# Optimization experiments

Hardware: AMD Instinct MI355X
Metric: run time of the kernel (lower is better)

## Reference

```python
import jax, jax.numpy as jnp
import numpy as np

N = 40000      # nodes
E = 640000     # edges (before self-loops)
F_IN = 32      # num_node_features
H = 8          # n_heads
C = 16         # hidden_channels
G = 1000       # graphs in batch
M = 256        # MLP_neurons
NEG_SLOPE = 0.2


def setup_inputs() -> dict:
    key = jax.random.key(0)
    ks = jax.random.split(key, 24)
    d = {}
    d["x"] = jax.random.normal(ks[0], (N, F_IN), jnp.float32)
    d["edge_index"] = jax.random.randint(ks[1], (2, E), 0, N, dtype=jnp.int32)
    d["batch"] = jnp.sort(jax.random.randint(ks[2], (N,), 0, G, dtype=jnp.int32))
    dims = [F_IN, H * C, H * C]
    k = 3
    for i in range(3):
        fin = dims[i]
        s = 1.0 / np.sqrt(fin)
        d[f"W{i}"] = jax.random.normal(ks[k], (fin, H * C), jnp.float32) * s; k += 1
        d[f"b{i}"] = jnp.zeros((H * C,), jnp.float32)
        d[f"as{i}"] = jax.random.normal(ks[k], (H, C), jnp.float32) * (1.0 / np.sqrt(C)); k += 1
        d[f"ad{i}"] = jax.random.normal(ks[k], (H, C), jnp.float32) * (1.0 / np.sqrt(C)); k += 1
    d["fW0"] = jax.random.normal(ks[k], (H * C, M), jnp.float32) * (1.0 / np.sqrt(H * C)); k += 1
    d["fb0"] = jnp.zeros((M,), jnp.float32)
    d["fW1"] = jax.random.normal(ks[k], (M, M), jnp.float32) * (1.0 / np.sqrt(M)); k += 1
    d["fb1"] = jnp.zeros((M,), jnp.float32)
    d["oW"] = jax.random.normal(ks[k], (M, 2), jnp.float32) * (1.0 / np.sqrt(M)); k += 1
    d["ob"] = jnp.zeros((2,), jnp.float32)
    return d


def _gat_layer(x, W, b, a_src, a_dst, src, dst):
    # x: [N, Fin] -> h: [N, H, C]
    h = (x @ W).reshape(N, H, C)
    al_src = jnp.einsum('nhc,hc->nh', h, a_src)   # [N, H]
    al_dst = jnp.einsum('nhc,hc->nh', h, a_dst)   # [N, H]
    # edge-wise attention logits (gather), LeakyReLU
    e = jax.nn.leaky_relu(al_src[src] + al_dst[dst], NEG_SLOPE)  # [E', H]
    # softmax over incoming edges of each dst node
    emax = jax.ops.segment_max(e, dst, num_segments=N)           # [N, H]
    ex = jnp.exp(e - emax[dst])
    denom = jax.ops.segment_sum(ex, dst, num_segments=N)         # [N, H]
    alpha = ex / denom[dst]
    # weighted scatter-aggregation of source features
    out = jax.ops.segment_sum(alpha[:, :, None] * h[src], dst, num_segments=N)  # [N, H, C]
    return out.reshape(N, H * C) + b


def reference(x, edge_index, batch, W0, b0, as0, ad0, W1, b1, as1, ad1,
              W2, b2, as2, ad2, fW0, fb0, fW1, fb1, oW, ob):
    # PyG GATConv adds self-loops by default
    loops = jnp.arange(N, dtype=edge_index.dtype)
    src = jnp.concatenate([edge_index[0], loops])
    dst = jnp.concatenate([edge_index[1], loops])
    h = x
    for (W, b, a_s, a_d) in ((W0, b0, as0, ad0), (W1, b1, as1, ad1), (W2, b2, as2, ad2)):
        h = jax.nn.relu(_gat_layer(h, W, b, a_s, a_d, src, dst))
    # global mean pool per graph
    sums = jax.ops.segment_sum(h, batch, num_segments=G)                    # [G, H*C]
    cnts = jax.ops.segment_sum(jnp.ones((N,), h.dtype), batch, num_segments=G)
    g = sums / jnp.maximum(cnts, 1.0)[:, None]
    # MLP head (dropout is identity in eval mode)
    g = jax.nn.relu(g @ fW0 + fb0)
    g = jax.nn.relu(g @ fW1 + fb1)
    return g @ oW + ob
```

## Files before the change

kernel.cpp:

```cpp
#include <hip/hip_runtime.h>
#include <hip/hip_fp16.h>
#include <math.h>

#define NN 40000
#define EE 640000
#define EP 680000
#define FIN0 32
#define HC 128
#define GG 1000
#define MM 256
#define SCAN_BLOCKS ((NN + 255) / 256)


__global__ void hist_kernel(const int* __restrict__ ei, int* __restrict__ deg,
                            int* __restrict__ rank) {
    int idx = blockIdx.x * 256 + threadIdx.x;
    if (idx >= EP) return;
    int d = (idx < EE) ? ei[EE + idx] : (idx - EE);
    rank[idx] = atomicAdd(&deg[d], 1);
}

__global__ __launch_bounds__(256) void scan_partial(const int* __restrict__ deg,
                                                    int* __restrict__ part) {
    int b = blockIdx.x, t = threadIdx.x;
    int i = b * 256 + t;
    int v = (i < NN) ? deg[i] : 0;
#pragma unroll
    for (int d = 1; d < 64; d <<= 1) v += __shfl_xor(v, d);
    __shared__ int ws[4];
    if ((t & 63) == 0) ws[t >> 6] = v;
    __syncthreads();
    if (t == 0) part[b] = ws[0] + ws[1] + ws[2] + ws[3];
}

__global__ __launch_bounds__(256) void scan_final(const int* __restrict__ deg,
                                                  const int* __restrict__ part,
                                                  int* __restrict__ offs) {
    int b = blockIdx.x, t = threadIdx.x;
    __shared__ int sbase;
    if (t < 64) {
        int s = 0;
        for (int l = t; l < b; l += 64) s += part[l];
#pragma unroll
        for (int d = 1; d < 64; d <<= 1) s += __shfl_xor(s, d);
        if (t == 0) sbase = s;
    }
    int i = b * 256 + t;
    int v = (i < NN) ? deg[i] : 0;
    __shared__ int tmp[256];
    tmp[t] = v;
    __syncthreads();
    for (int st = 1; st < 256; st <<= 1) {
        int add = (t >= st) ? tmp[t - st] : 0;
        __syncthreads();
        tmp[t] += add;
        __syncthreads();
    }
    int excl = tmp[t] - v + sbase;
    if (i < NN) offs[i] = excl;
    if (i == NN - 1) offs[NN] = excl + v;
}

__global__ void scatter_kernel(const int* __restrict__ ei, const int* __restrict__ offs,
                               const int* __restrict__ rank, int* __restrict__ esrc) {
    int idx = blockIdx.x * 256 + threadIdx.x;
    if (idx >= EP) return;
    int s, d;
    if (idx < EE) { s = ei[idx]; d = ei[EE + idx]; } else { s = idx - EE; d = s; }
    esrc[offs[d] + rank[idx]] = s;
}


template <int FIN>
__global__ __launch_bounds__(256) void proj_kernel(const float* __restrict__ X,
                                                   const float* __restrict__ W,
                                                   const float* __restrict__ a_src,
                                                   const float* __restrict__ a_dst,
                                                   __half* __restrict__ H2,
                                                   float* __restrict__ als,
                                                   float* __restrict__ ald) {
    constexpr int KT = 32;
    static_assert(FIN % KT == 0, "FIN % KT");
    __shared__ float xs[KT][68];
    __shared__ float ws[KT][128];
    int t = threadIdx.x;
    int node0 = blockIdx.x * 64;
    int nt = t & 15;
    int ct = t >> 4;
    float acc[4][8];
#pragma unroll
    for (int i = 0; i < 4; i++)
#pragma unroll
        for (int j = 0; j < 8; j++) acc[i][j] = 0.f;

    for (int kk = 0; kk < FIN; kk += KT) {
#pragma unroll
        for (int r = 0; r < (64 * KT) / 256; r++) {
            int idx = r * 256 + t;
            int n = idx / KT, k = idx % KT;
            xs[k][n] = X[(node0 + n) * FIN + kk + k];
        }
#pragma unroll
        for (int r = 0; r < (KT * 128) / 256; r++) {
            int idx = r * 256 + t;
            int k = idx >> 7, c = idx & 127;
            ws[k][c] = W[(kk + k) * 128 + c];
        }
        __syncthreads();
#pragma unroll
        for (int k = 0; k < KT; k++) {
            const float4 xv = *(const float4*)(&xs[k][4 * nt]);
            const float4 wa = *(const float4*)(&ws[k][8 * ct]);
            const float4 wb = *(const float4*)(&ws[k][8 * ct + 4]);
            float xr[4] = {xv.x, xv.y, xv.z, xv.w};
            float wr[8] = {wa.x, wa.y, wa.z, wa.w, wb.x, wb.y, wb.z, wb.w};
#pragma unroll
            for (int i = 0; i < 4; i++)
#pragma unroll
                for (int j = 0; j < 8; j++) acc[i][j] = fmaf(xr[i], wr[j], acc[i][j]);
        }
        __syncthreads();
    }
#pragma unroll
    for (int i = 0; i < 4; i++) {
        int n = node0 + 4 * nt + i;
        __half2 p0 = __floats2half2_rn(acc[i][0], acc[i][1]);
        __half2 p1 = __floats2half2_rn(acc[i][2], acc[i][3]);
        __half2 p2 = __floats2half2_rn(acc[i][4], acc[i][5]);
        __half2 p3 = __floats2half2_rn(acc[i][6], acc[i][7]);
        uint4 pk;
        pk.x = *(unsigned*)&p0; pk.y = *(unsigned*)&p1;
        pk.z = *(unsigned*)&p2; pk.w = *(unsigned*)&p3;
        *(uint4*)(&H2[(size_t)n * HC + 8 * ct]) = pk;
    }
    float sa[4] = {0.f, 0.f, 0.f, 0.f}, da[4] = {0.f, 0.f, 0.f, 0.f};
#pragma unroll
    for (int j = 0; j < 8; j++) {
        float av = a_src[ct * 8 + j];
        float dv = a_dst[ct * 8 + j];
#pragma unroll
        for (int i = 0; i < 4; i++) {
            sa[i] = fmaf(acc[i][j], av, sa[i]);
            da[i] = fmaf(acc[i][j], dv, da[i]);
        }
    }
#pragma unroll
    for (int i = 0; i < 4; i++) {
        sa[i] += __shfl_xor(sa[i], 16);
        da[i] += __shfl_xor(da[i], 16);
    }
    if ((ct & 1) == 0) {
        int head = ct >> 1;
#pragma unroll
        for (int i = 0; i < 4; i++) {
            int n = node0 + 4 * nt + i;
            als[n * 8 + head] = sa[i];
            ald[n * 8 + head] = da[i];
        }
    }
}


__global__ __launch_bounds__(256) void agg_kernel(const __half* __restrict__ H2,
                                                  const float* __restrict__ als,
                                                  const float* __restrict__ ald,
                                                  const int* __restrict__ offs,
                                                  const int* __restrict__ esrc,
                                                  const float* __restrict__ bias,
                                                  float* __restrict__ OUT) {
    int t = threadIdx.x;
    int n = blockIdx.x * 4 + (t >> 6);
    int t6 = t & 63;
    int c8 = t6 & 15;
    int slot = (t6 >> 4) & 3;
    int hd = c8 >> 1;
    int beg = offs[n], end = offs[n + 1];
    float ad = ald[n * 8 + hd];
    float acc[8] = {0.f, 0.f, 0.f, 0.f, 0.f, 0.f, 0.f, 0.f};
    float denom = 0.f;
    const float4* H4 = (const float4*)H2;

    int p = beg + slot;
    int s_cur = 0; float al_cur = 0.f;
    if (p < end) {
        s_cur = esrc[p];
        al_cur = als[s_cur * 8 + hd];
    }
#pragma unroll 2
    while (p < end) {
        int pn = p + 4;
        int s_nxt = 0;
        if (pn < end) s_nxt = esrc[pn];
        float x = al_cur + ad;
        x = (x > 0.f) ? x : 0.2f * x;
        float w = __expf(x);
        float4 r = H4[(size_t)s_cur * 16 + c8];
        float al_nxt = 0.f;
        if (pn < end) al_nxt = als[s_nxt * 8 + hd];
        __half2 h0 = *(__half2*)&r.x;
        __half2 h1 = *(__half2*)&r.y;
        __half2 h2 = *(__half2*)&r.z;
        __half2 h3 = *(__half2*)&r.w;
        float2 f0 = __half22float2(h0);
        float2 f1 = __half22float2(h1);
        float2 f2 = __half22float2(h2);
        float2 f3 = __half22float2(h3);
        acc[0] = fmaf(w, f0.x, acc[0]); acc[1] = fmaf(w, f0.y, acc[1]);
        acc[2] = fmaf(w, f1.x, acc[2]); acc[3] = fmaf(w, f1.y, acc[3]);
        acc[4] = fmaf(w, f2.x, acc[4]); acc[5] = fmaf(w, f2.y, acc[5]);
        acc[6] = fmaf(w, f3.x, acc[6]); acc[7] = fmaf(w, f3.y, acc[7]);
        denom += w;
        s_cur = s_nxt; al_cur = al_nxt;
        p = pn;
    }
#pragma unroll
    for (int j = 0; j < 8; j++) {
        acc[j] += __shfl_xor(acc[j], 16);
        acc[j] += __shfl_xor(acc[j], 32);
    }
    denom += __shfl_xor(denom, 16);
    denom += __shfl_xor(denom, 32);
    if (slot == 0 && t6 < 16) {
        float inv = 1.0f / denom;
        const float4 ba = ((const float4*)bias)[2 * c8];
        const float4 bb = ((const float4*)bias)[2 * c8 + 1];
        float4 o0, o1;
        o0.x = fmaxf(fmaf(acc[0], inv, ba.x), 0.f);
        o0.y = fmaxf(fmaf(acc[1], inv, ba.y), 0.f);
        o0.z = fmaxf(fmaf(acc[2], inv, ba.z), 0.f);
        o0.w = fmaxf(fmaf(acc[3], inv, ba.w), 0.f);
        o1.x = fmaxf(fmaf(acc[4], inv, bb.x), 0.f);
        o1.y = fmaxf(fmaf(acc[5], inv, bb.y), 0.f);
        o1.z = fmaxf(fmaf(acc[6], inv, bb.z), 0.f);
        o1.w = fmaxf(fmaf(acc[7], inv, bb.w), 0.f);
        ((float4*)OUT)[(size_t)n * 32 + 2 * c8]     = o0;
        ((float4*)OUT)[(size_t)n * 32 + 2 * c8 + 1] = o1;
    }
}


__global__ __launch_bounds__(256) void mlp_fused(const float* __restrict__ B,
                                                 const int* __restrict__ batch,
                                                 const float* __restrict__ fW0,
                                                 const float* __restrict__ fb0,
                                                 const float* __restrict__ fW1,
                                                 const float* __restrict__ fb1,
                                                 const float* __restrict__ oW,
                                                 const float* __restrict__ ob,
                                                 float* __restrict__ out) {
    __shared__ int lo[3];
    __shared__ float rows[2][128];
    __shared__ float g1s[2][256];
    __shared__ float g2s[2][256];
    int t = threadIdx.x;
    int g0 = blockIdx.x * 2;
    if (t < 3) {
        int target = g0 + t;
        int a = 0, b = NN;
        while (a < b) { int mid = (a + b) >> 1; if (batch[mid] < target) a = mid + 1; else b = mid; }
        lo[t] = a;
    }
    __syncthreads();
    {
        int j = t >> 7, c = t & 127;
        int s0 = lo[j], s1 = lo[j + 1];
        float s = 0.f;
        float p0 = 0.f, p1 = 0.f, p2 = 0.f, p3 = 0.f;
        int n = s0;
        for (; n + 3 < s1; n += 4) {
            p0 += B[(size_t)n * 128 + c];
            p1 += B[(size_t)(n + 1) * 128 + c];
            p2 += B[(size_t)(n + 2) * 128 + c];
            p3 += B[(size_t)(n + 3) * 128 + c];
        }
        for (; n < s1; n++) s += B[(size_t)n * 128 + c];
        s += (p0 + p1) + (p2 + p3);
        rows[j][c] = s / fmaxf((float)(s1 - s0), 1.0f);
    }
    __syncthreads();
    float a0 = 0.f, a1 = 0.f;
#pragma unroll 8
    for (int k = 0; k < 128; k++) {
        float w = fW0[k * 256 + t];
        a0 = fmaf(rows[0][k], w, a0);
        a1 = fmaf(rows[1][k], w, a1);
    }
    float b0v = fb0[t];
    g1s[0][t] = fmaxf(a0 + b0v, 0.f);
    g1s[1][t] = fmaxf(a1 + b0v, 0.f);
    __syncthreads();
    a0 = 0.f; a1 = 0.f;
#pragma unroll 8
    for (int k = 0; k < 256; k++) {
        float w = fW1[k * 256 + t];
        a0 = fmaf(g1s[0][k], w, a0);
        a1 = fmaf(g1s[1][k], w, a1);
    }
    float b1v = fb1[t];
    g2s[0][t] = fmaxf(a0 + b1v, 0.f);
    g2s[1][t] = fmaxf(a1 + b1v, 0.f);
    __syncthreads();
    if (t < 64) {
        int jj = t >> 5, l = t & 31;
        float p0 = 0.f, p1 = 0.f;
#pragma unroll
        for (int k = l; k < 256; k += 32) {
            float v = g2s[jj][k];
            p0 = fmaf(v, oW[k * 2 + 0], p0);
            p1 = fmaf(v, oW[k * 2 + 1], p1);
        }
#pragma unroll
        for (int d = 1; d < 32; d <<= 1) {
            p0 += __shfl_xor(p0, d);
            p1 += __shfl_xor(p1, d);
        }
        if (l == 0) {
            out[(g0 + jj) * 2 + 0] = p0 + ob[0];
            out[(g0 + jj) * 2 + 1] = p1 + ob[1];
        }
    }
}


extern "C" void kernel_launch(void* const* d_in, const int* in_sizes, int n_in,
                              void* d_out, int out_size, void* d_ws, size_t ws_size,
                              hipStream_t stream) {
    const float* x    = (const float*)d_in[0];
    const int* ei     = (const int*)d_in[1];
    const int* batch  = (const int*)d_in[2];
    const float* W[3]   = {(const float*)d_in[3], (const float*)d_in[7],  (const float*)d_in[11]};
    const float* bs[3]  = {(const float*)d_in[4], (const float*)d_in[8],  (const float*)d_in[12]};
    const float* asr[3] = {(const float*)d_in[5], (const float*)d_in[9],  (const float*)d_in[13]};
    const float* adt[3] = {(const float*)d_in[6], (const float*)d_in[10], (const float*)d_in[14]};
    const float* fW0 = (const float*)d_in[15];
    const float* fb0 = (const float*)d_in[16];
    const float* fW1 = (const float*)d_in[17];
    const float* fb1 = (const float*)d_in[18];
    const float* oW  = (const float*)d_in[19];
    const float* ob  = (const float*)d_in[20];
    float* out = (float*)d_out;

    char* base = (char*)d_ws;
    size_t off = 0;
    auto alloc = [&](size_t bytes) -> void* {
        void* p = base + off;
        off += (bytes + 255) & ~(size_t)255;
        return p;
    };
    int* deg    = (int*)alloc((size_t)NN * 4);
    int* offs   = (int*)alloc((size_t)(NN + 1) * 4);
    int* part   = (int*)alloc((size_t)SCAN_BLOCKS * 4);
    int* rank   = (int*)alloc((size_t)EP * 4);
    int* esrc   = (int*)alloc((size_t)EP * 4);
    __half* H2  = (__half*)alloc((size_t)NN * HC * 2);
    float* B    = (float*)alloc((size_t)NN * HC * 4);
    float* als  = (float*)alloc((size_t)NN * 8 * 4);
    float* ald  = (float*)alloc((size_t)NN * 8 * 4);

    hipMemsetAsync(deg, 0, (size_t)NN * 4, stream);

    hist_kernel<<<(EP + 255) / 256, 256, 0, stream>>>(ei, deg, rank);
    scan_partial<<<SCAN_BLOCKS, 256, 0, stream>>>(deg, part);
    scan_final<<<SCAN_BLOCKS, 256, 0, stream>>>(deg, part, offs);
    scatter_kernel<<<(EP + 255) / 256, 256, 0, stream>>>(ei, offs, rank, esrc);

    const float* cur = x;
    for (int l = 0; l < 3; l++) {
        if (l == 0) proj_kernel<FIN0><<<NN / 64, 256, 0, stream>>>(cur, W[l], asr[l], adt[l], H2, als, ald);
        else        proj_kernel<HC><<<NN / 64, 256, 0, stream>>>(cur, W[l], asr[l], adt[l], H2, als, ald);
        agg_kernel<<<NN / 4, 256, 0, stream>>>(H2, als, ald, offs, esrc, bs[l], B);
        cur = B;
    }
    mlp_fused<<<GG / 2, 256, 0, stream>>>(B, batch, fW0, fb0, fW1, fb1, oW, ob, out);
}
```

Baseline: 319.7 us.

## Use fp16 MFMA for hidden-layer projections and fuse layer-0 proj with histogram

Replaces the fp32 FMA projection for layers 1 and 2 with an MFMA 16x16x32 fp16 kernel. It reads fp16 activations written by the aggregation kernel, which now emits half output for the first two layers, and uses pre-transposed fp16 weights. The layer-0 projection, the degree histogram and the weight transpose/convert are merged into one prep kernel launch, so independent work overlaps and there are fewer launches. This lowers the precision of the intermediate activations and weights to fp16 and halves the activation bytes written and read between layers.

```diff
diff --git a/kernel.cpp b/kernel.cpp
--- a/kernel.cpp
+++ b/kernel.cpp
@@ -10,81 +10,53 @@
 #define GG 1000
 #define MM 256
 #define SCAN_BLOCKS ((NN + 255) / 256)
-
-
-__global__ void hist_kernel(const int* __restrict__ ei, int* __restrict__ deg,
-                            int* __restrict__ rank) {
-    int idx = blockIdx.x * 256 + threadIdx.x;
-    if (idx >= EP) return;
-    int d = (idx < EE) ? ei[EE + idx] : (idx - EE);
-    rank[idx] = atomicAdd(&deg[d], 1);
-}
-
-__global__ __launch_bounds__(256) void scan_partial(const int* __restrict__ deg,
-                                                    int* __restrict__ part) {
-    int b = blockIdx.x, t = threadIdx.x;
-    int i = b * 256 + t;
-    int v = (i < NN) ? deg[i] : 0;
-#pragma unroll
-    for (int d = 1; d < 64; d <<= 1) v += __shfl_xor(v, d);
-    __shared__ int ws[4];
-    if ((t & 63) == 0) ws[t >> 6] = v;
-    __syncthreads();
-    if (t == 0) part[b] = ws[0] + ws[1] + ws[2] + ws[3];
-}
-
-__global__ __launch_bounds__(256) void scan_final(const int* __restrict__ deg,
-                                                  const int* __restrict__ part,
-                                                  int* __restrict__ offs) {
-    int b = blockIdx.x, t = threadIdx.x;
-    __shared__ int sbase;
-    if (t < 64) {
-        int s = 0;
-        for (int l = t; l < b; l += 64) s += part[l];
-#pragma unroll
-        for (int d = 1; d < 64; d <<= 1) s += __shfl_xor(s, d);
-        if (t == 0) sbase = s;
-    }
-    int i = b * 256 + t;
-    int v = (i < NN) ? deg[i] : 0;
-    __shared__ int tmp[256];
-    tmp[t] = v;
-    __syncthreads();
-    for (int st = 1; st < 256; st <<= 1) {
-        int add = (t >= st) ? tmp[t - st] : 0;
-        __syncthreads();
-        tmp[t] += add;
-        __syncthreads();
-    }
-    int excl = tmp[t] - v + sbase;
-    if (i < NN) offs[i] = excl;
-    if (i == NN - 1) offs[NN] = excl + v;
-}
-
-__global__ void scatter_kernel(const int* __restrict__ ei, const int* __restrict__ offs,
-                               const int* __restrict__ rank, int* __restrict__ esrc) {
-    int idx = blockIdx.x * 256 + threadIdx.x;
-    if (idx >= EP) return;
-    int s, d;
-    if (idx < EE) { s = ei[idx]; d = ei[EE + idx]; } else { s = idx - EE; d = s; }
-    esrc[offs[d] + rank[idx]] = s;
-}
-
-
-template <int FIN>
-__global__ __launch_bounds__(256) void proj_kernel(const float* __restrict__ X,
-                                                   const float* __restrict__ W,
+#define PROJ0_BLOCKS (NN / 64)
+#define HIST_BLOCKS ((EP + 255) / 256)
+#define PADH 136
+
+typedef _Float16 f16x8 __attribute__((ext_vector_type(8)));
+typedef float f32x4 __attribute__((ext_vector_type(4)));
+
+
+__global__ __launch_bounds__(256) void prep_kernel(const float* __restrict__ X,
+                                                   const float* __restrict__ W0,
                                                    const float* __restrict__ a_src,
                                                    const float* __restrict__ a_dst,
                                                    __half* __restrict__ H2,
                                                    float* __restrict__ als,
-                                                   float* __restrict__ ald) {
-    constexpr int KT = 32;
-    static_assert(FIN % KT == 0, "FIN % KT");
-    __shared__ float xs[KT][68];
-    __shared__ float ws[KT][128];
+                                                   float* __restrict__ ald,
+                                                   const int* __restrict__ ei,
+                                                   int* __restrict__ deg,
+                                                   int* __restrict__ rank,
+                                                   const float* __restrict__ W1,
+                                                   const float* __restrict__ W2,
+                                                   __half* __restrict__ Wt1,
+                                                   __half* __restrict__ Wt2) {
     int t = threadIdx.x;
-    int node0 = blockIdx.x * 64;
+    int b = blockIdx.x;
+    if (b >= PROJ0_BLOCKS && b < PROJ0_BLOCKS + HIST_BLOCKS) {
+        int idx = (b - PROJ0_BLOCKS) * 256 + t;
+        if (idx < EP) {
+            int d = (idx < EE) ? ei[EE + idx] : (idx - EE);
+            rank[idx] = atomicAdd(&deg[d], 1);
+        }
+        return;
+    }
+    if (b >= PROJ0_BLOCKS + HIST_BLOCKS) {
+        int l = b - (PROJ0_BLOCKS + HIST_BLOCKS);
+        const float* Wsrc = (l == 0) ? W1 : W2;
+        __half* Wd = (l == 0) ? Wt1 : Wt2;
+#pragma unroll 8
+        for (int r = 0; r < 64; r++) {
+            int idx = r * 256 + t;
+            int k = idx >> 7, c = idx & 127;
+            Wd[c * 128 + k] = __float2half(Wsrc[idx]);
+        }
+        return;
+    }
+    __shared__ float xs[32][68];
+    __shared__ float ws[32][128];
+    int node0 = b * 64;
     int nt = t & 15;
     int ct = t >> 4;
     float acc[4][8];
@@ -92,34 +64,30 @@
     for (int i = 0; i < 4; i++)
 #pragma unroll
         for (int j = 0; j < 8; j++) acc[i][j] = 0.f;
-
-    for (int kk = 0; kk < FIN; kk += KT) {
-#pragma unroll
-        for (int r = 0; r < (64 * KT) / 256; r++) {
-            int idx = r * 256 + t;
-            int n = idx / KT, k = idx % KT;
-            xs[k][n] = X[(node0 + n) * FIN + kk + k];
-        }
-#pragma unroll
-        for (int r = 0; r < (KT * 128) / 256; r++) {
-            int idx = r * 256 + t;
-            int k = idx >> 7, c = idx & 127;
-            ws[k][c] = W[(kk + k) * 128 + c];
-        }
-        __syncthreads();
-#pragma unroll
-        for (int k = 0; k < KT; k++) {
-            const float4 xv = *(const float4*)(&xs[k][4 * nt]);
-            const float4 wa = *(const float4*)(&ws[k][8 * ct]);
-            const float4 wb = *(const float4*)(&ws[k][8 * ct + 4]);
-            float xr[4] = {xv.x, xv.y, xv.z, xv.w};
-            float wr[8] = {wa.x, wa.y, wa.z, wa.w, wb.x, wb.y, wb.z, wb.w};
-#pragma unroll
-            for (int i = 0; i < 4; i++)
-#pragma unroll
-                for (int j = 0; j < 8; j++) acc[i][j] = fmaf(xr[i], wr[j], acc[i][j]);
-        }
-        __syncthreads();
+#pragma unroll
+    for (int r = 0; r < 8; r++) {
+        int idx = r * 256 + t;
+        int n = idx >> 5, k = idx & 31;
+        xs[k][n] = X[(node0 + n) * FIN0 + k];
+    }
+#pragma unroll
+    for (int r = 0; r < 16; r++) {
+        int idx = r * 256 + t;
+        int k = idx >> 7, c = idx & 127;
+        ws[k][c] = W0[k * 128 + c];
+    }
+    __syncthreads();
+#pragma unroll
+    for (int k = 0; k < 32; k++) {
+        const float4 xv = *(const float4*)(&xs[k][4 * nt]);
+        const float4 wa = *(const float4*)(&ws[k][8 * ct]);
+        const float4 wb = *(const float4*)(&ws[k][8 * ct + 4]);
+        float xr[4] = {xv.x, xv.y, xv.z, xv.w};
+        float wr[8] = {wa.x, wa.y, wa.z, wa.w, wb.x, wb.y, wb.z, wb.w};
+#pragma unroll
+        for (int i = 0; i < 4; i++)
+#pragma unroll
+            for (int j = 0; j < 8; j++) acc[i][j] = fmaf(xr[i], wr[j], acc[i][j]);
     }
 #pragma unroll
     for (int i = 0; i < 4; i++) {
@@ -161,13 +129,168 @@
 }
 
 
+__global__ __launch_bounds__(256) void scan_partial(const int* __restrict__ deg,
+                                                    int* __restrict__ part) {
+    int b = blockIdx.x, t = threadIdx.x;
+    int i = b * 256 + t;
+    int v = (i < NN) ? deg[i] : 0;
+#pragma unroll
+    for (int d = 1; d < 64; d <<= 1) v += __shfl_xor(v, d);
+    __shared__ int ws[4];
+    if ((t & 63) == 0) ws[t >> 6] = v;
+    __syncthreads();
+    if (t == 0) part[b] = ws[0] + ws[1] + ws[2] + ws[3];
+}
+
+__global__ __launch_bounds__(256) void scan_final(const int* __restrict__ deg,
+                                                  const int* __restrict__ part,
+                                                  int* __restrict__ offs) {
+    int b = blockIdx.x, t = threadIdx.x;
+    __shared__ int sbase;
+    if (t < 64) {
+        int s = 0;
+        for (int l = t; l < b; l += 64) s += part[l];
+#pragma unroll
+        for (int d = 1; d < 64; d <<= 1) s += __shfl_xor(s, d);
+        if (t == 0) sbase = s;
+    }
+    int i = b * 256 + t;
+    int v = (i < NN) ? deg[i] : 0;
+    __shared__ int tmp[256];
+    tmp[t] = v;
+    __syncthreads();
+    for (int st = 1; st < 256; st <<= 1) {
+        int add = (t >= st) ? tmp[t - st] : 0;
+        __syncthreads();
+        tmp[t] += add;
+        __syncthreads();
+    }
+    int excl = tmp[t] - v + sbase;
+    if (i < NN) offs[i] = excl;
+    if (i == NN - 1) offs[NN] = excl + v;
+}
+
+__global__ void scatter_kernel(const int* __restrict__ ei, const int* __restrict__ offs,
+                               const int* __restrict__ rank, int* __restrict__ esrc) {
+    int idx = blockIdx.x * 256 + threadIdx.x;
+    if (idx >= EP) return;
+    int s, d;
+    if (idx < EE) { s = ei[idx]; d = ei[EE + idx]; } else { s = idx - EE; d = s; }
+    esrc[offs[d] + rank[idx]] = s;
+}
+
+
+__global__ __launch_bounds__(256) void proj_mfma(const __half* __restrict__ Bin,
+                                                 const __half* __restrict__ Wt,
+                                                 const float* __restrict__ a_src,
+                                                 const float* __restrict__ a_dst,
+                                                 __half* __restrict__ H2,
+                                                 float* __restrict__ als,
+                                                 float* __restrict__ ald) {
+    __shared__ __half As[64 * PADH];
+    __shared__ __half Ws[128 * PADH];
+    int t = threadIdx.x;
+    int node0 = blockIdx.x * 64;
+    {
+        int n = t >> 2, kk = (t & 3) * 32;
+        const uint4* src = (const uint4*)(&Bin[(size_t)(node0 + n) * 128 + kk]);
+        uint4 v0 = src[0];
+        uint4 v1 = src[1];
+        uint4 v2 = src[2];
+        uint4 v3 = src[3];
+        uint4* dst = (uint4*)(&As[n * PADH + kk]);
+        dst[0] = v0; dst[1] = v1; dst[2] = v2; dst[3] = v3;
+    }
+#pragma unroll
+    for (int r = 0; r < 8; r++) {
+        int idx = r * 256 + t;
+        int c = idx >> 4;
+        int kk = (idx & 15) * 8;
+        uint4 v = *(const uint4*)(&Wt[c * 128 + kk]);
+        *(uint4*)(&Ws[c * PADH + kk]) = v;
+    }
+    __syncthreads();
+    int w = t >> 6, l = t & 63;
+    int lr = l & 15, lg = l >> 4;
+    f32x4 acc[8];
+    f32x4 z4 = {0.f, 0.f, 0.f, 0.f};
+#pragma unroll
+    for (int n = 0; n < 8; n++) acc[n] = z4;
+    const __half* arow = &As[(16 * w + lr) * PADH + lg * 8];
+#pragma unroll
+    for (int ks = 0; ks < 4; ks++) {
+        f16x8 af = *(const f16x8*)(arow + 32 * ks);
+#pragma unroll
+        for (int n = 0; n < 8; n++) {
+            f16x8 bf = *(const f16x8*)(&Ws[(16 * n + lr) * PADH + lg * 8 + 32 * ks]);
+            acc[n] = __builtin_amdgcn_mfma_f32_16x16x32_f16(af, bf, acc[n], 0, 0, 0);
+        }
+    }
+#pragma unroll
+    for (int n = 0; n < 8; n++)
+#pragma unroll
+        for (int j = 0; j < 4; j++)
+            As[(16 * w + lg * 4 + j) * PADH + 16 * n + lr] = __float2half(acc[n][j]);
+    __syncthreads();
+    {
+        int n = t >> 2, kk = (t & 3) * 32;
+        const uint4* src = (const uint4*)(&As[n * PADH + kk]);
+        uint4 v0 = src[0];
+        uint4 v1 = src[1];
+        uint4 v2 = src[2];
+        uint4 v3 = src[3];
+        uint4* dst = (uint4*)(&H2[(size_t)(node0 + n) * 128 + kk]);
+        dst[0] = v0; dst[1] = v1; dst[2] = v2; dst[3] = v3;
+    }
+    {
+        int nt = t & 15, ct = t >> 4;
+        float av[8], dv[8];
+#pragma unroll
+        for (int j = 0; j < 8; j++) { av[j] = a_src[ct * 8 + j]; dv[j] = a_dst[ct * 8 + j]; }
+        float sa[4], da[4];
+#pragma unroll
+        for (int i = 0; i < 4; i++) {
+            uint4 hv = *(const uint4*)(&As[(4 * nt + i) * PADH + 8 * ct]);
+            __half2 h0 = *(__half2*)&hv.x;
+            __half2 h1 = *(__half2*)&hv.y;
+            __half2 h2 = *(__half2*)&hv.z;
+            __half2 h3 = *(__half2*)&hv.w;
+            float2 f0 = __half22float2(h0);
+            float2 f1 = __half22float2(h1);
+            float2 f2 = __half22float2(h2);
+            float2 f3 = __half22float2(h3);
+            sa[i] = f0.x * av[0] + f0.y * av[1] + f1.x * av[2] + f1.y * av[3] +
+                    f2.x * av[4] + f2.y * av[5] + f3.x * av[6] + f3.y * av[7];
+            da[i] = f0.x * dv[0] + f0.y * dv[1] + f1.x * dv[2] + f1.y * dv[3] +
+                    f2.x * dv[4] + f2.y * dv[5] + f3.x * dv[6] + f3.y * dv[7];
+        }
+#pragma unroll
+        for (int i = 0; i < 4; i++) {
+            sa[i] += __shfl_xor(sa[i], 16);
+            da[i] += __shfl_xor(da[i], 16);
+        }
+        if ((ct & 1) == 0) {
+            int head = ct >> 1;
+#pragma unroll
+            for (int i = 0; i < 4; i++) {
+                int n = node0 + 4 * nt + i;
+                als[n * 8 + head] = sa[i];
+                ald[n * 8 + head] = da[i];
+            }
+        }
+    }
+}
+
+
+template <bool HALF_OUT>
 __global__ __launch_bounds__(256) void agg_kernel(const __half* __restrict__ H2,
                                                   const float* __restrict__ als,
                                                   const float* __restrict__ ald,
                                                   const int* __restrict__ offs,
                                                   const int* __restrict__ esrc,
                                                   const float* __restrict__ bias,
-                                                  float* __restrict__ OUT) {
+                                                  float* __restrict__ OUT,
+                                                  __half* __restrict__ OUT2) {
     int t = threadIdx.x;
     int n = blockIdx.x * 4 + (t >> 6);
     int t6 = t & 63;
@@ -224,17 +347,30 @@
         float inv = 1.0f / denom;
         const float4 ba = ((const float4*)bias)[2 * c8];
         const float4 bb = ((const float4*)bias)[2 * c8 + 1];
-        float4 o0, o1;
-        o0.x = fmaxf(fmaf(acc[0], inv, ba.x), 0.f);
-        o0.y = fmaxf(fmaf(acc[1], inv, ba.y), 0.f);
-        o0.z = fmaxf(fmaf(acc[2], inv, ba.z), 0.f);
-        o0.w = fmaxf(fmaf(acc[3], inv, ba.w), 0.f);
-        o1.x = fmaxf(fmaf(acc[4], inv, bb.x), 0.f);
-        o1.y = fmaxf(fmaf(acc[5], inv, bb.y), 0.f);
-        o1.z = fmaxf(fmaf(acc[6], inv, bb.z), 0.f);
-        o1.w = fmaxf(fmaf(acc[7], inv, bb.w), 0.f);
-        ((float4*)OUT)[(size_t)n * 32 + 2 * c8]     = o0;
-        ((float4*)OUT)[(size_t)n * 32 + 2 * c8 + 1] = o1;
+        float o0 = fmaxf(fmaf(acc[0], inv, ba.x), 0.f);
+        float o1 = fmaxf(fmaf(acc[1], inv, ba.y), 0.f);
+        float o2 = fmaxf(fmaf(acc[2], inv, ba.z), 0.f);
+        float o3 = fmaxf(fmaf(acc[3], inv, ba.w), 0.f);
+        float o4 = fmaxf(fmaf(acc[4], inv, bb.x), 0.f);
+        float o5 = fmaxf(fmaf(acc[5], inv, bb.y), 0.f);
+        float o6 = fmaxf(fmaf(acc[6], inv, bb.z), 0.f);
+        float o7 = fmaxf(fmaf(acc[7], inv, bb.w), 0.f);
+        if (HALF_OUT) {
+            __half2 q0 = __floats2half2_rn(o0, o1);
+            __half2 q1 = __floats2half2_rn(o2, o3);
+            __half2 q2 = __floats2half2_rn(o4, o5);
+            __half2 q3 = __floats2half2_rn(o6, o7);
+            uint4 pk;
+            pk.x = *(unsigned*)&q0; pk.y = *(unsigned*)&q1;
+            pk.z = *(unsigned*)&q2; pk.w = *(unsigned*)&q3;
+            ((uint4*)OUT2)[(size_t)n * 16 + c8] = pk;
+        } else {
+            float4 v0, v1;
+            v0.x = o0; v0.y = o1; v0.z = o2; v0.w = o3;
+            v1.x = o4; v1.y = o5; v1.z = o6; v1.w = o7;
+            ((float4*)OUT)[(size_t)n * 32 + 2 * c8]     = v0;
+            ((float4*)OUT)[(size_t)n * 32 + 2 * c8 + 1] = v1;
+        }
     }
 }
 
@@ -354,22 +490,25 @@
     int* esrc   = (int*)alloc((size_t)EP * 4);
     __half* H2  = (__half*)alloc((size_t)NN * HC * 2);
     float* B    = (float*)alloc((size_t)NN * HC * 4);
+    __half* B2  = (__half*)alloc((size_t)NN * HC * 2);
     float* als  = (float*)alloc((size_t)NN * 8 * 4);
     float* ald  = (float*)alloc((size_t)NN * 8 * 4);
+    __half* Wt1 = (__half*)alloc((size_t)HC * HC * 2);
+    __half* Wt2 = (__half*)alloc((size_t)HC * HC * 2);
 
     hipMemsetAsync(deg, 0, (size_t)NN * 4, stream);
 
-    hist_kernel<<<(EP + 255) / 256, 256, 0, stream>>>(ei, deg, rank);
+    prep_kernel<<<PROJ0_BLOCKS + HIST_BLOCKS + 2, 256, 0, stream>>>(
+        x, W[0], asr[0], adt[0], H2, als, ald, ei, deg, rank, W[1], W[2], Wt1, Wt2);
     scan_partial<<<SCAN_BLOCKS, 256, 0, stream>>>(deg, part);
     scan_final<<<SCAN_BLOCKS, 256, 0, stream>>>(deg, part, offs);
     scatter_kernel<<<(EP + 255) / 256, 256, 0, stream>>>(ei, offs, rank, esrc);
 
-    const float* cur = x;
-    for (int l = 0; l < 3; l++) {
-        if (l == 0) proj_kernel<FIN0><<<NN / 64, 256, 0, stream>>>(cur, W[l], asr[l], adt[l], H2, als, ald);
-        else        proj_kernel<HC><<<NN / 64, 256, 0, stream>>>(cur, W[l], asr[l], adt[l], H2, als, ald);
-        agg_kernel<<<NN / 4, 256, 0, stream>>>(H2, als, ald, offs, esrc, bs[l], B);
-        cur = B;
-    }
+    agg_kernel<true><<<NN / 4, 256, 0, stream>>>(H2, als, ald, offs, esrc, bs[0], nullptr, B2);
+    proj_mfma<<<PROJ0_BLOCKS, 256, 0, stream>>>(B2, Wt1, asr[1], adt[1], H2, als, ald);
+    agg_kernel<true><<<NN / 4, 256, 0, stream>>>(H2, als, ald, offs, esrc, bs[1], nullptr, B2);
+    proj_mfma<<<PROJ0_BLOCKS, 256, 0, stream>>>(B2, Wt2, asr[2], adt[2], H2, als, ald);
+    agg_kernel<false><<<NN / 4, 256, 0, stream>>>(H2, als, ald, offs, esrc, bs[2], B, nullptr);
+
     mlp_fused<<<GG / 2, 256, 0, stream>>>(B, batch, fW0, fb0, fW1, fb1, oW, ob, out);
 }
```

After: 295.4 us (median of 2 runs). -7.6%, faster.
